# Performance work log

Hardware: AMD Instinct MI355X
Metric: run time of the kernel (lower is better)

Reference implementation:

```python
import jax, jax.numpy as jnp
import numpy as np

C_IN, C_OUT, GROUPS = 1024, 1024, 8
H, W_SP = 256, 256


def _block_diag_mask():
    # group-conv sparsity pattern: block-diagonal [C_out, C_in] boolean mask
    blk = jnp.ones((C_OUT // GROUPS, C_IN // GROUPS), dtype=jnp.float32)
    return jnp.kron(jnp.eye(GROUPS, dtype=jnp.float32), blk) > 0


def setup_inputs() -> dict:
    key = jax.random.key(0)
    k1, k2 = jax.random.split(key)
    x = jax.random.normal(k1, (1, C_IN, H, W_SP), dtype=jnp.float32)
    W = jax.random.normal(k2, (C_OUT, C_IN), dtype=jnp.float32)
    mask = _block_diag_mask()  # constant sparsity pattern (nnz = C_in*C_out/groups)
    return {"x": x, "W": W, "mask": mask}


def reference(x, W, mask):
    # SparseGroupConv2d.forward: y = sparse_W @ x.view(C_in, H*W), viewed back
    h, w = x.shape[2], x.shape[3]
    x_ = x.reshape(C_IN, h * w)                      # [C_in, P]
    W_sp = jnp.where(mask, W, 0.0)                   # masked weight == sparse COO values
    y_ = jnp.matmul(W_sp, x_)                        # [C_out, P]
    return y_.reshape(1, C_OUT, h, w)
```

## Files before the change

kernel.cpp:

```cpp
#include <hip/hip_runtime.h>
#include <hip/hip_bf16.h>


#define GC   128
#define CIN  1024
#define PT   65536
#define BN   256

typedef __attribute__((ext_vector_type(8))) short bf16x8;
typedef __attribute__((ext_vector_type(4))) float f32x4;

__device__ __forceinline__ unsigned short f2bf(float f) {
    union { float f; unsigned int u; } v; v.f = f;
    unsigned int r = v.u + 0x7FFF + ((v.u >> 16) & 1);
    return (unsigned short)(r >> 16);
}

__global__ __launch_bounds__(256) void sparse_group_conv_kernel(
        const float* __restrict__ x, const float* __restrict__ w,
        float* __restrict__ y) {
    __shared__ unsigned short Wlds[GC * GC];

    const int t = threadIdx.x;
    const int g = blockIdx.y;
    const int p_blk = blockIdx.x * BN;

    {
        const float* Wg = w + (g * GC) * CIN + g * GC;
        const int mbase = t >> 5;
        const int k = (t & 31) * 4;
        #pragma unroll
        for (int it = 0; it < 16; ++it) {
            const int mm = it * 8 + mbase;
            const float4 w4 = *reinterpret_cast<const float4*>(Wg + mm * CIN + k);
            ushort4 h;
            h.x = f2bf(w4.x); h.y = f2bf(w4.y); h.z = f2bf(w4.z); h.w = f2bf(w4.w);
            const int idx = (mm * GC + k) ^ ((mm & 7) << 3);
            *reinterpret_cast<ushort4*>(&Wlds[idx]) = h;
        }
    }
    __syncthreads();

    const int lane = t & 63;
    const int wv   = t >> 6;
    const int r    = lane & 15;
    const int q    = lane >> 4;

    const float* Xg = x + (g * GC) * PT;
    float*       Yg = y + (g * GC) * PT;

    #pragma unroll
    for (int c = 0; c < 4; ++c) {
        const int p = p_blk + wv * 64 + c * 16 + r;

        f32x4 acc[8];
        #pragma unroll
        for (int mi = 0; mi < 8; ++mi) acc[mi] = (f32x4){0.f, 0.f, 0.f, 0.f};

        #pragma unroll
        for (int ks = 0; ks < 4; ++ks) {
            const float* xp = Xg + (ks * 32 + q * 8) * PT + p;
            float xb[8];
            #pragma unroll
            for (int j = 0; j < 8; ++j) xb[j] = xp[j * PT];
            bf16x8 b;
            #pragma unroll
            for (int j = 0; j < 8; ++j) b[j] = (short)f2bf(xb[j]);

            #pragma unroll
            for (int mi = 0; mi < 8; ++mi) {
                const int mrow = mi * 16 + r;
                const int idx = (mrow * GC + ks * 32 + q * 8) ^ ((mrow & 7) << 3);
                const bf16x8 a = *reinterpret_cast<const bf16x8*>(&Wlds[idx]);
                acc[mi] = __builtin_amdgcn_mfma_f32_16x16x32_bf16(a, b, acc[mi], 0, 0, 0);
            }
        }

        float* yp = Yg + p;
        #pragma unroll
        for (int mi = 0; mi < 8; ++mi) {
            #pragma unroll
            for (int rr = 0; rr < 4; ++rr) {
                yp[(mi * 16 + q * 4 + rr) * PT] = acc[mi][rr];
            }
        }
    }
}

extern "C" void kernel_launch(void* const* d_in, const int* in_sizes, int n_in,
                              void* d_out, int out_size, void* d_ws, size_t ws_size,
                              hipStream_t stream) {
    const float* x = (const float*)d_in[0];
    const float* w = (const float*)d_in[1];
    float* y = (float*)d_out;

    dim3 grid(PT / BN, 8);
    dim3 block(256);
    sparse_group_conv_kernel<<<grid, block, 0, stream>>>(x, w, y);
}
```

Measured before the change: 498.8 us.

## Stage X tile through LDS with coalesced float4 loads and halve pixel tile

Instead of each lane gathering scalar X values strided by PT straight from global memory, the block now loads a 128x128 X tile with coalesced float4 reads, converts it to bf16 into padded LDS, and builds MFMA B fragments from LDS. X and W global loads are issued up front into registers before conversion, so more memory requests are in flight at once. The pixel tile per block shrinks from 256 to 128, doubling the grid and re-reading the W slice more often, while each wave now computes two 16-column MFMA groups that share each A fragment. Register pressure rises from holding 32 float4 values, and the 2-byte strided LDS reads for B may hit bank conflicts.

```diff
diff --git a/kernel.cpp b/kernel.cpp
--- a/kernel.cpp
+++ b/kernel.cpp
@@ -5,7 +5,8 @@
 #define GC   128
 #define CIN  1024
 #define PT   65536
-#define BN   256
+#define BN   128
+#define XLD  132
 
 typedef __attribute__((ext_vector_type(8))) short bf16x8;
 typedef __attribute__((ext_vector_type(4))) float f32x4;
@@ -20,24 +21,49 @@
         const float* __restrict__ x, const float* __restrict__ w,
         float* __restrict__ y) {
     __shared__ unsigned short Wlds[GC * GC];
+    __shared__ unsigned short Xlds[GC * XLD];
 
-    const int t = threadIdx.x;
-    const int g = blockIdx.y;
-    const int p_blk = blockIdx.x * BN;
+    const int t  = threadIdx.x;
+    const int g  = blockIdx.y;
+    const int p0 = blockIdx.x * BN;
 
-    {
-        const float* Wg = w + (g * GC) * CIN + g * GC;
-        const int mbase = t >> 5;
+    const float* Xg = x + (size_t)(g * GC) * PT + p0;
+    const float* Wg = w + (size_t)(g * GC) * CIN + g * GC;
+
+    float4 xr[16];
+    #pragma unroll
+    for (int it = 0; it < 16; ++it) {
+        const int f = it * 256 + t;
+        const int row = f >> 5;
+        const int m = f & 31;
+        xr[it] = *reinterpret_cast<const float4*>(Xg + (size_t)row * PT + 4 * m);
+    }
+    float4 wr[16];
+    #pragma unroll
+    for (int it = 0; it < 16; ++it) {
+        const int mm = it * 8 + (t >> 5);
+        wr[it] = *reinterpret_cast<const float4*>(Wg + (size_t)mm * CIN + (t & 31) * 4);
+    }
+
+    #pragma unroll
+    for (int it = 0; it < 16; ++it) {
+        const int f = it * 256 + t;
+        const int row = f >> 5;
+        const int m = f & 31;
+        ushort4 h;
+        h.x = f2bf(xr[it].x); h.y = f2bf(xr[it].y);
+        h.z = f2bf(xr[it].z); h.w = f2bf(xr[it].w);
+        *reinterpret_cast<ushort4*>(&Xlds[row * XLD + 4 * m]) = h;
+    }
+    #pragma unroll
+    for (int it = 0; it < 16; ++it) {
+        const int mm = it * 8 + (t >> 5);
         const int k = (t & 31) * 4;
-        #pragma unroll
-        for (int it = 0; it < 16; ++it) {
-            const int mm = it * 8 + mbase;
-            const float4 w4 = *reinterpret_cast<const float4*>(Wg + mm * CIN + k);
-            ushort4 h;
-            h.x = f2bf(w4.x); h.y = f2bf(w4.y); h.z = f2bf(w4.z); h.w = f2bf(w4.w);
-            const int idx = (mm * GC + k) ^ ((mm & 7) << 3);
-            *reinterpret_cast<ushort4*>(&Wlds[idx]) = h;
-        }
+        ushort4 h;
+        h.x = f2bf(wr[it].x); h.y = f2bf(wr[it].y);
+        h.z = f2bf(wr[it].z); h.w = f2bf(wr[it].w);
+        const int idx = (mm * GC + k) ^ ((mm & 7) << 3);
+        *reinterpret_cast<ushort4*>(&Wlds[idx]) = h;
     }
     __syncthreads();
 
@@ -46,42 +72,45 @@
     const int r    = lane & 15;
     const int q    = lane >> 4;
 
-    const float* Xg = x + (g * GC) * PT;
-    float*       Yg = y + (g * GC) * PT;
+    f32x4 acc[2][8];
+    #pragma unroll
+    for (int pg = 0; pg < 2; ++pg)
+        #pragma unroll
+        for (int mi = 0; mi < 8; ++mi)
+            acc[pg][mi] = (f32x4){0.f, 0.f, 0.f, 0.f};
 
     #pragma unroll
-    for (int c = 0; c < 4; ++c) {
-        const int p = p_blk + wv * 64 + c * 16 + r;
+    for (int ks = 0; ks < 4; ++ks) {
+        bf16x8 b[2];
+        #pragma unroll
+        for (int pg = 0; pg < 2; ++pg) {
+            const int px = wv * 32 + pg * 16 + r;
+            const unsigned short* col = &Xlds[(ks * 32 + q * 8) * XLD + px];
+            short tmp[8];
+            #pragma unroll
+            for (int j = 0; j < 8; ++j) tmp[j] = (short)col[j * XLD];
+            b[pg] = (bf16x8){tmp[0], tmp[1], tmp[2], tmp[3],
+                             tmp[4], tmp[5], tmp[6], tmp[7]};
+        }
+        #pragma unroll
+        for (int mi = 0; mi < 8; ++mi) {
+            const int mrow = mi * 16 + r;
+            const int idx = (mrow * GC + ks * 32 + q * 8) ^ ((mrow & 7) << 3);
+            const bf16x8 a = *reinterpret_cast<const bf16x8*>(&Wlds[idx]);
+            acc[0][mi] = __builtin_amdgcn_mfma_f32_16x16x32_bf16(a, b[0], acc[0][mi], 0, 0, 0);
+            acc[1][mi] = __builtin_amdgcn_mfma_f32_16x16x32_bf16(a, b[1], acc[1][mi], 0, 0, 0);
+        }
+    }
 
-        f32x4 acc[8];
-        #pragma unroll
-        for (int mi = 0; mi < 8; ++mi) acc[mi] = (f32x4){0.f, 0.f, 0.f, 0.f};
-
-        #pragma unroll
-        for (int ks = 0; ks < 4; ++ks) {
-            const float* xp = Xg + (ks * 32 + q * 8) * PT + p;
-            float xb[8];
-            #pragma unroll
-            for (int j = 0; j < 8; ++j) xb[j] = xp[j * PT];
-            bf16x8 b;
-            #pragma unroll
-            for (int j = 0; j < 8; ++j) b[j] = (short)f2bf(xb[j]);
-
-            #pragma unroll
-            for (int mi = 0; mi < 8; ++mi) {
-                const int mrow = mi * 16 + r;
-                const int idx = (mrow * GC + ks * 32 + q * 8) ^ ((mrow & 7) << 3);
-                const bf16x8 a = *reinterpret_cast<const bf16x8*>(&Wlds[idx]);
-                acc[mi] = __builtin_amdgcn_mfma_f32_16x16x32_bf16(a, b, acc[mi], 0, 0, 0);
-            }
-        }
-
-        float* yp = Yg + p;
+    float* Yg = y + (size_t)(g * GC) * PT + p0;
+    #pragma unroll
+    for (int pg = 0; pg < 2; ++pg) {
+        float* yp = Yg + wv * 32 + pg * 16 + r;
         #pragma unroll
         for (int mi = 0; mi < 8; ++mi) {
             #pragma unroll
             for (int rr = 0; rr < 4; ++rr) {
-                yp[(mi * 16 + q * 4 + rr) * PT] = acc[mi][rr];
+                yp[(size_t)(mi * 16 + q * 4 + rr) * PT] = acc[pg][mi][rr];
             }
         }
     }
```

New measurement: 456.5 us. -8.5%, faster.

## Pre-convert weights to bf16 in a prep kernel and stage X tiles through LDS

Applied to the files above, without the earlier changes.

A separate prep kernel now converts each group's diagonal weight block to swizzled bf16 once, and the main kernel copies it into LDS with plain vector loads instead of reconverting fp32 weights in every block. The X tile is loaded with coalesced float4 reads, converted to bf16 and kept in a padded LDS buffer, so strided per-lane scalar global loads are no longer needed. The pixel tile per block drops from 256 to 64, which raises the block count and the number of times the weight block is reloaded from L2. The change also adds a second kernel launch and uses the workspace buffer.

```diff
diff --git a/kernel.cpp b/kernel.cpp
--- a/kernel.cpp
+++ b/kernel.cpp
@@ -5,39 +5,73 @@
 #define GC   128
 #define CIN  1024
 #define PT   65536
-#define BN   256
+#define BN   64
+#define XLD  68
+#define WG_ELEMS (GC * GC)
 
 typedef __attribute__((ext_vector_type(8))) short bf16x8;
 typedef __attribute__((ext_vector_type(4))) float f32x4;
 
 __device__ __forceinline__ unsigned short f2bf(float f) {
-    union { float f; unsigned int u; } v; v.f = f;
-    unsigned int r = v.u + 0x7FFF + ((v.u >> 16) & 1);
-    return (unsigned short)(r >> 16);
+    __hip_bfloat16 h = __float2bfloat16(f);
+    return *reinterpret_cast<unsigned short*>(&h);
+}
+
+__global__ __launch_bounds__(256) void wprep_kernel(
+        const float* __restrict__ w, unsigned short* __restrict__ wf) {
+    const int b = blockIdx.x;
+    const int g = b >> 3, s = b & 7;
+    const int t = threadIdx.x;
+    const int mm = s * 16 + (t >> 4);
+    const int k  = (t & 15) * 8;
+    const float* src = w + (size_t)(g * GC + mm) * CIN + g * GC + k;
+    const float4 w0 = *reinterpret_cast<const float4*>(src);
+    const float4 w1 = *reinterpret_cast<const float4*>(src + 4);
+    ushort4 h0, h1;
+    h0.x = f2bf(w0.x); h0.y = f2bf(w0.y); h0.z = f2bf(w0.z); h0.w = f2bf(w0.w);
+    h1.x = f2bf(w1.x); h1.y = f2bf(w1.y); h1.z = f2bf(w1.z); h1.w = f2bf(w1.w);
+    const int idx = (mm * GC + k) ^ ((mm & 7) << 3);
+    unsigned short* dst = wf + (size_t)g * WG_ELEMS + idx;
+    *reinterpret_cast<ushort4*>(dst)     = h0;
+    *reinterpret_cast<ushort4*>(dst + 4) = h1;
 }
 
 __global__ __launch_bounds__(256) void sparse_group_conv_kernel(
-        const float* __restrict__ x, const float* __restrict__ w,
+        const float* __restrict__ x, const unsigned short* __restrict__ wf,
         float* __restrict__ y) {
     __shared__ unsigned short Wlds[GC * GC];
+    __shared__ unsigned short Xlds[GC * XLD];
 
-    const int t = threadIdx.x;
-    const int g = blockIdx.y;
-    const int p_blk = blockIdx.x * BN;
+    const int t  = threadIdx.x;
+    const int g  = blockIdx.y;
+    const int p0 = blockIdx.x * BN;
 
-    {
-        const float* Wg = w + (g * GC) * CIN + g * GC;
-        const int mbase = t >> 5;
-        const int k = (t & 31) * 4;
-        #pragma unroll
-        for (int it = 0; it < 16; ++it) {
-            const int mm = it * 8 + mbase;
-            const float4 w4 = *reinterpret_cast<const float4*>(Wg + mm * CIN + k);
-            ushort4 h;
-            h.x = f2bf(w4.x); h.y = f2bf(w4.y); h.z = f2bf(w4.z); h.w = f2bf(w4.w);
-            const int idx = (mm * GC + k) ^ ((mm & 7) << 3);
-            *reinterpret_cast<ushort4*>(&Wlds[idx]) = h;
-        }
+    const unsigned short* wsrc = wf + (size_t)g * WG_ELEMS + t * 8;
+    uint4 wr[8];
+    #pragma unroll
+    for (int it = 0; it < 8; ++it)
+        wr[it] = *reinterpret_cast<const uint4*>(wsrc + it * 2048);
+
+    const float* Xg = x + (size_t)(g * GC) * PT + p0;
+    float4 xr[8];
+    #pragma unroll
+    for (int it = 0; it < 8; ++it) {
+        const int f_i = it * 256 + t;
+        const int row = f_i >> 4, m = f_i & 15;
+        xr[it] = *reinterpret_cast<const float4*>(Xg + (size_t)row * PT + 4 * m);
+    }
+
+    #pragma unroll
+    for (int it = 0; it < 8; ++it)
+        *reinterpret_cast<uint4*>(&Wlds[t * 8 + it * 2048]) = wr[it];
+    #pragma unroll
+    for (int it = 0; it < 8; ++it) {
+        const int f_i = it * 256 + t;
+        const int row = f_i >> 4, m = f_i & 15;
+        ushort4 h;
+        h.x = f2bf(xr[it].x); h.y = f2bf(xr[it].y);
+        h.z = f2bf(xr[it].z); h.w = f2bf(xr[it].w);
+        *reinterpret_cast<ushort4*>(&Xlds[row * XLD + 4 * m]) = h;
     }
     __syncthreads();
 
@@ -45,44 +79,35 @@
     const int wv   = t >> 6;
     const int r    = lane & 15;
     const int q    = lane >> 4;
+    const int px   = wv * 16 + r;
 
-    const float* Xg = x + (g * GC) * PT;
-    float*       Yg = y + (g * GC) * PT;
+    f32x4 acc[8];
+    #pragma unroll
+    for (int mi = 0; mi < 8; ++mi) acc[mi] = (f32x4){0.f, 0.f, 0.f, 0.f};
 
     #pragma unroll
-    for (int c = 0; c < 4; ++c) {
-        const int p = p_blk + wv * 64 + c * 16 + r;
-
-        f32x4 acc[8];
+    for (int ks = 0; ks < 4; ++ks) {
+        const unsigned short* col = &Xlds[(ks * 32 + q * 8) * XLD + px];
+        short tmp[8];
         #pragma unroll
-        for (int mi = 0; mi < 8; ++mi) acc[mi] = (f32x4){0.f, 0.f, 0.f, 0.f};
-
-        #pragma unroll
-        for (int ks = 0; ks < 4; ++ks) {
-            const float* xp = Xg + (ks * 32 + q * 8) * PT + p;
-            float xb[8];
-            #pragma unroll
-            for (int j = 0; j < 8; ++j) xb[j] = xp[j * PT];
-            bf16x8 b;
-            #pragma unroll
-            for (int j = 0; j < 8; ++j) b[j] = (short)f2bf(xb[j]);
-
-            #pragma unroll
-            for (int mi = 0; mi < 8; ++mi) {
-                const int mrow = mi * 16 + r;
-                const int idx = (mrow * GC + ks * 32 + q * 8) ^ ((mrow & 7) << 3);
-                const bf16x8 a = *reinterpret_cast<const bf16x8*>(&Wlds[idx]);
-                acc[mi] = __builtin_amdgcn_mfma_f32_16x16x32_bf16(a, b, acc[mi], 0, 0, 0);
-            }
-        }
-
-        float* yp = Yg + p;
+        for (int j = 0; j < 8; ++j) tmp[j] = (short)col[j * XLD];
+        const bf16x8 b = (bf16x8){tmp[0], tmp[1], tmp[2], tmp[3],
+                                  tmp[4], tmp[5], tmp[6], tmp[7]};
         #pragma unroll
         for (int mi = 0; mi < 8; ++mi) {
-            #pragma unroll
-            for (int rr = 0; rr < 4; ++rr) {
-                yp[(mi * 16 + q * 4 + rr) * PT] = acc[mi][rr];
-            }
+            const int mrow = mi * 16 + r;
+            const int idx = (mrow * GC + ks * 32 + q * 8) ^ ((mrow & 7) << 3);
+            const bf16x8 a = *reinterpret_cast<const bf16x8*>(&Wlds[idx]);
+            acc[mi] = __builtin_amdgcn_mfma_f32_16x16x32_bf16(a, b, acc[mi], 0, 0, 0);
+        }
+    }
+
+    float* yp = y + (size_t)(g * GC) * PT + p0 + px;
+    #pragma unroll
+    for (int mi = 0; mi < 8; ++mi) {
+        #pragma unroll
+        for (int rr = 0; rr < 4; ++rr) {
+            yp[(size_t)(mi * 16 + q * 4 + rr) * PT] = acc[mi][rr];
         }
     }
 }
@@ -93,8 +118,9 @@
     const float* x = (const float*)d_in[0];
     const float* w = (const float*)d_in[1];
     float* y = (float*)d_out;
+    unsigned short* wf = (unsigned short*)d_ws;
 
+    wprep_kernel<<<dim3(64), dim3(256), 0, stream>>>(w, wf);
     dim3 grid(PT / BN, 8);
-    dim3 block(256);
-    sparse_group_conv_kernel<<<grid, block, 0, stream>>>(x, w, y);
+    sparse_group_conv_kernel<<<grid, dim3(256), 0, stream>>>(x, wf, y);
 }
```

Result: faster. 447.8 us (-10.2%).
